# Kernel optimization log

Measured on AMD Instinct MI355X. Metric: run time of the kernel, lower is better.

## Reference

```python
import jax, jax.numpy as jnp
import numpy as np

NUM_LEVELS = 4
RADIUS = 4
B, C, H, W = 2, 256, 96, 96


def _grid_sample_abs(img, grid):
    """Bilinear sample with absolute pixel coords, align_corners=True, zero padding.

    img:  (N, h, w)
    grid: (N, K, K, 2) with last dim = (x, y) absolute pixel coordinates.
    Returns (N, K, K).
    """
    h, w = img.shape[-2:]
    x = grid[..., 0]
    y = grid[..., 1]
    x0 = jnp.floor(x)
    y0 = jnp.floor(y)
    wx1 = x - x0
    wy1 = y - y0
    wx0 = 1.0 - wx1
    wy0 = 1.0 - wy1
    n = jnp.arange(img.shape[0])[:, None, None]

    def gather(xi, yi):
        valid = (xi >= 0) & (xi <= w - 1) & (yi >= 0) & (yi <= h - 1)
        xc = jnp.clip(xi, 0, w - 1).astype(jnp.int32)
        yc = jnp.clip(yi, 0, h - 1).astype(jnp.int32)
        return jnp.where(valid, img[n, yc, xc], 0.0)

    return (gather(x0, y0) * wx0 * wy0
            + gather(x0 + 1, y0) * wx1 * wy0
            + gather(x0, y0 + 1) * wx0 * wy1
            + gather(x0 + 1, y0 + 1) * wx1 * wy1)


def _avg_pool2(x):
    # x: (N, h, w) -> (N, h//2, w//2), kernel 2 stride 2
    n, h, w = x.shape
    return x.reshape(n, h // 2, 2, w // 2, 2).mean(axis=(2, 4))


def setup_inputs() -> dict:
    key = jax.random.key(0)
    k1, k2, k3 = jax.random.split(key, 3)
    fmap1 = jax.random.normal(k1, (B, C, H, W), dtype=jnp.float32)
    fmap2 = jax.random.normal(k2, (B, C, H, W), dtype=jnp.float32)
    # absolute pixel coords (x, y) within the feature map
    centroids_coords = jax.random.uniform(k3, (B, 2, H, W), dtype=jnp.float32) * (W - 1)
    return {"fmap1": fmap1, "fmap2": fmap2, "centroids_coords": centroids_coords}


def reference(fmap1, fmap2, centroids_coords):
    b, c, h, w = fmap1.shape
    # all-pairs dot-product correlation volume: (B, HW, HW)
    f1 = fmap1.reshape(b, c, h * w)
    f2 = fmap2.reshape(b, c, h * w)
    corr = jnp.einsum('bcp,bcq->bpq', f1, f2) / jnp.sqrt(jnp.float32(c))
    corr = corr.reshape(b * h * w, h, w)

    pyramid = [corr]
    for _ in range(NUM_LEVELS - 1):
        corr = _avg_pool2(corr)
        pyramid.append(corr)

    k = 2 * RADIUS + 1
    di = jnp.linspace(-RADIUS, RADIUS, k, dtype=jnp.float32)
    dij = jnp.stack(jnp.meshgrid(di, di, indexing='ij'), axis=-1)  # (k, k, 2)
    delta = dij.reshape(1, k, k, 2)

    cent = centroids_coords.transpose(0, 2, 3, 1).reshape(b * h * w, 1, 1, 2)
    feats = []
    for lvl in pyramid:
        coords = cent + delta                      # (BHW, k, k, 2)
        sampled = _grid_sample_abs(lvl, coords)    # (BHW, k, k)
        feats.append(sampled.reshape(b, h, w, k * k))
        cent = cent / 2

    out = jnp.concatenate(feats, axis=-1)          # (B, H, W, num_levels*k*k)
    return out.transpose(0, 3, 1, 2)
```

## Files before the change

### kernel.cpp

```cpp
#include <hip/hip_runtime.h>
#include <stdint.h>

#define B_ 2
#define C_ 256
#define H_ 96
#define W_ 96
#define HW_ (H_*W_)

typedef _Float16 half8 __attribute__((ext_vector_type(8)));
typedef float f32x4 __attribute__((ext_vector_type(4)));

#define ZPOFF   0u
#define CNTOFF  512u
#define PERMOFF 4096u
#define F1OFF   225280u
#define L0OFF   9662464u
#define L1OFF   19099648u
#define L2OFF   21458944u
#define L3OFF   22048768u
#define SCROFF  22196224u

#define CAP 96
#define DLW 226

__global__ __launch_bounds__(256) void k_tr2(const float* __restrict__ f1,
                                             const float* __restrict__ f2,
                                             _Float16* __restrict__ f1t,
                                             _Float16* __restrict__ L0h) {
  __shared__ float t[32][33];
  const int z = blockIdx.z;
  const int b = z & 1;
  const bool is2 = (z >> 1) != 0;
  const float* in = is2 ? f2 : f1;
  _Float16* out = is2 ? L0h : f1t;
  const float scale = is2 ? 1.0f : 0.0625f;

  const int p0 = blockIdx.x * 32, c0 = blockIdx.y * 32;
  const int tx = threadIdx.x, ty = threadIdx.y;
  const float* src = in + ((size_t)b * C_ + c0) * HW_ + p0;
#pragma unroll
  for (int i = 0; i < 4; ++i)
    t[ty + 8 * i][tx] = src[(size_t)(ty + 8 * i) * HW_ + tx];
  __syncthreads();
  _Float16* dst = out + ((size_t)b * HW_ + p0) * C_ + c0;
#pragma unroll
  for (int i = 0; i < 4; ++i)
    dst[(size_t)(ty + 8 * i) * C_ + tx] = (_Float16)(t[tx][ty + 8 * i] * scale);
}

__global__ __launch_bounds__(256) void k_pool3(const _Float16* __restrict__ L0,
                                               _Float16* __restrict__ L1,
                                               _Float16* __restrict__ L2,
                                               _Float16* __restrict__ L3) {
  int idx = blockIdx.x;
  const int X = idx % 12; idx /= 12;
  const int Y = idx % 12; const int b = idx / 12;
  const int c = threadIdx.x;

  const _Float16* base = L0 + (((size_t)b * 96 + 8 * Y) * 96 + 8 * X) * C_ + c;
  float s1[4][4];
#pragma unroll
  for (int i = 0; i < 4; ++i)
#pragma unroll
    for (int j = 0; j < 4; ++j) {
      const _Float16* p = base + ((size_t)(2 * i) * 96 + 2 * j) * C_;
      s1[i][j] = ((float)p[0] + (float)p[C_] +
                  (float)p[96 * C_] + (float)p[96 * C_ + C_]) * 0.25f;
    }
#pragma unroll
  for (int i = 0; i < 4; ++i)
#pragma unroll
    for (int j = 0; j < 4; ++j)
      L1[(((size_t)b * 48 + 4 * Y + i) * 48 + 4 * X + j) * C_ + c] = (_Float16)s1[i][j];

  float s2[2][2];
#pragma unroll
  for (int i = 0; i < 2; ++i)
#pragma unroll
    for (int j = 0; j < 2; ++j) {
      s2[i][j] = (s1[2 * i][2 * j] + s1[2 * i][2 * j + 1] +
                  s1[2 * i + 1][2 * j] + s1[2 * i + 1][2 * j + 1]) * 0.25f;
      L2[(((size_t)b * 24 + 2 * Y + i) * 24 + 2 * X + j) * C_ + c] = (_Float16)s2[i][j];
    }

  const float s3 = (s2[0][0] + s2[0][1] + s2[1][0] + s2[1][1]) * 0.25f;
  L3[(((size_t)b * 12 + Y) * 12 + X) * C_ + c] = (_Float16)s3;
}

__global__ __launch_bounds__(256) void k_bucket(const float* __restrict__ cent,
                                                int* __restrict__ cnt,
                                                int* __restrict__ perm) {
  const int t = blockIdx.x * 256 + threadIdx.x;
  const int b = t / HW_, yx = t - b * HW_;
  const float cx = cent[(size_t)b * 2 * HW_ + yx];
  const float cy = cent[(size_t)b * 2 * HW_ + HW_ + yx];
  int ci = (int)(cx * 0.125f); ci = min(max(ci, 0), 11);
  int cj = (int)(cy * 0.25f);  cj = min(max(cj, 0), 23);
  const int cell = b * 288 + cj * 12 + ci;
  const int pos = atomicAdd(&cnt[cell], 1);
  if (pos < CAP) perm[cell * CAP + pos] = t;
}

template <int LVL>
__device__ __forceinline__ void cell_level(char* __restrict__ ws,
                                           const float* __restrict__ cent,
                                           int b, int ci, int cj,
                                           const int* __restrict__ pc, int npix,
                                           _Float16* __restrict__ dl,
                                           float* __restrict__ prm, int lane) {
  constexpr int wl = 96 >> LVL;
  constexpr int Wx = (LVL == 0) ? 17 : (LVL == 1) ? 13 : (LVL == 2) ? 11 : 10;
  constexpr int Hy = (LVL == 0) ? 13 : (LVL == 1) ? 11 : 10;
  constexpr int N = Wx * Hy;
  constexpr int ntiles = (N + 15) >> 4;
  constexpr uint32_t LB = (LVL == 0) ? L0OFF : (LVL == 1) ? L1OFF
                        : (LVL == 2) ? L2OFF : L3OFF;
  constexpr uint32_t PBl = (LVL == 0) ? 4718592u : (LVL == 1) ? 1179648u
                         : (LVL == 2) ? 294912u : 73728u;
  constexpr float inv = 1.0f / (float)(1 << LVL);

  const int FXl = (LVL == 0) ? (ci << 3) : (LVL == 1) ? (ci << 2)
                : (LVL == 2) ? (ci << 1) : ci;
  const int FYl = (LVL == 0) ? (cj << 2) : (LVL == 1) ? (cj << 1)
                : (LVL == 2) ? cj : (cj >> 1);
  const int XW0 = FXl - 4, YW0 = FYl - 4;
  const char* lbase = ws + LB + (size_t)b * PBl;
  const char* zp = ws + ZPOFF;
  const char* f1b = ws + F1OFF;
  char* scrb = ws + SCROFF;

  const int row16 = lane & 15, kb = lane >> 4;
  const int nmt = (npix + 47) / 48;

  for (int mt = 0; mt < nmt; ++mt) {
    const int rem = npix - mt * 48;
    const int remc = min(rem, 48);

    half8 av0[8], av1[8], av2[8];
    {
      const int i0 = mt * 48 + row16;
      const int pv0 = (i0 < npix) ? pc[i0] : pc[0];
      const char* a0 = f1b + (size_t)pv0 * 512 + kb * 16;
#pragma unroll
      for (int k = 0; k < 8; ++k) av0[k] = *(const half8*)(a0 + k * 64);
    }
    if (rem > 16) {
      const int i1 = mt * 48 + 16 + row16;
      const int pv1 = (i1 < npix) ? pc[i1] : pc[0];
      const char* a1 = f1b + (size_t)pv1 * 512 + kb * 16;
#pragma unroll
      for (int k = 0; k < 8; ++k) av1[k] = *(const half8*)(a1 + k * 64);
    }
    if (rem > 32) {
      const int i2 = mt * 48 + 32 + row16;
      const int pv2 = (i2 < npix) ? pc[i2] : pc[0];
      const char* a2 = f1b + (size_t)pv2 * 512 + kb * 16;
#pragma unroll
      for (int k = 0; k < 8; ++k) av2[k] = *(const half8*)(a2 + k * 64);
    }

    if (lane < remc) {
      const int pv = pc[mt * 48 + lane];
      const int yx = pv - b * HW_;
      const float cx = cent[(size_t)b * 2 * HW_ + yx];
      const float cy = cent[(size_t)b * 2 * HW_ + HW_ + yx];
      const float cxl = cx * inv, cyl = cy * inv;
      const float fxl = floorf(cxl), fyl = floorf(cyl);
      const int sxp = (int)fxl - FXl, syp = (int)fyl - FYl;
      prm[lane * 4 + 0] = cxl - fxl;
      prm[lane * 4 + 1] = cyl - fyl;
      ((int*)prm)[lane * 4 + 2] = syp * Wx + sxp;
      ((int*)prm)[lane * 4 + 3] = pv;
    }

#pragma unroll
    for (int j = 0; j < ntiles; ++j) {
      const int n = j * 16 + row16;
      const int sy = n / Wx, sx = n - sy * Wx;
      const int gy = YW0 + sy, gx = XW0 + sx;
      const bool val = (n < N) & (gy >= 0) & (gy < wl) & (gx >= 0) & (gx < wl);
      const char* bp = (val ? (lbase + (((size_t)(gy * wl + gx)) << 9)) : zp)
                       + kb * 16;
      half8 bv[8];
#pragma unroll
      for (int k = 0; k < 8; ++k) bv[k] = *(const half8*)(bp + k * 64);

      f32x4 acc0 = {0.f, 0.f, 0.f, 0.f};
#pragma unroll
      for (int k = 0; k < 8; ++k)
        acc0 = __builtin_amdgcn_mfma_f32_16x16x32_f16(av0[k], bv[k], acc0, 0, 0, 0);
      const int col = j * 16 + row16;
#pragma unroll
      for (int j4 = 0; j4 < 4; ++j4)
        dl[(kb * 4 + j4) * DLW + col] = (_Float16)acc0[j4];

      if (rem > 16) {
        f32x4 acc1 = {0.f, 0.f, 0.f, 0.f};
#pragma unroll
        for (int k = 0; k < 8; ++k)
          acc1 = __builtin_amdgcn_mfma_f32_16x16x32_f16(av1[k], bv[k], acc1, 0, 0, 0);
#pragma unroll
        for (int j4 = 0; j4 < 4; ++j4)
          dl[(kb * 4 + j4 + 16) * DLW + col] = (_Float16)acc1[j4];
      }
      if (rem > 32) {
        f32x4 acc2 = {0.f, 0.f, 0.f, 0.f};
#pragma unroll
        for (int k = 0; k < 8; ++k)
          acc2 = __builtin_amdgcn_mfma_f32_16x16x32_f16(av2[k], bv[k], acc2, 0, 0, 0);
#pragma unroll
        for (int j4 = 0; j4 < 4; ++j4)
          dl[(kb * 4 + j4 + 32) * DLW + col] = (_Float16)acc2[j4];
      }
    }

    {
      const int total = remc * 41;
      for (int s = lane; s < total; s += 64) {
        const int p = s / 41;
        const int c = s - p * 41;
        const float wx1 = prm[p * 4 + 0];
        const float wy1 = prm[p * 4 + 1];
        const int n0 = ((const int*)prm)[p * 4 + 2];
        const int pv = ((const int*)prm)[p * 4 + 3];
        const float wx0 = 1.f - wx1, wy0 = 1.f - wy1;
        const _Float16* d = &dl[p * DLW];
        uint32_t packed = 0;
#pragma unroll
        for (int e = 0; e < 2; ++e) {
          const int o = 2 * c + e;
          const int a = o / 9, bq = o - a * 9;
          const int n = n0 + bq * Wx + a;
          const float d00 = (float)d[n],      d10 = (float)d[n + 1];
          const float d01 = (float)d[n + Wx], d11 = (float)d[n + Wx + 1];
          const float v = wy0 * (wx0 * d00 + wx1 * d10) +
                          wy1 * (wx0 * d01 + wx1 * d11);
          const _Float16 h = (_Float16)v;
          packed |= ((uint32_t)*(const uint16_t*)&h) << (16 * e);
        }
        *(uint32_t*)(scrb + (size_t)pv * 656 + LVL * 164 + c * 4) = packed;
      }
    }
  }
}

__global__ __launch_bounds__(64, 2) void k_cell(char* __restrict__ ws,
                                                const float* __restrict__ cent) {
  __shared__ _Float16 dl[48 * DLW];
  __shared__ float prm[48 * 4];

  const int bx = blockIdx.x;
  const int xcd = bx & 7, slot = bx >> 3;
  const int b = xcd >> 2, band = xcd & 3;
  const int lvl = slot / 72;
  const int rem = slot - lvl * 72;
  const int cjb = rem / 12, ci = rem - cjb * 12;
  const int cj = band * 6 + cjb;
  const int cell = b * 288 + cj * 12 + ci;

  const int* cnt = (const int*)(ws + CNTOFF);
  const int npix = min(cnt[cell], CAP);
  if (npix == 0) return;
  const int* pc = (const int*)(ws + PERMOFF) + cell * CAP;

  const int lane = threadIdx.x;
  switch (lvl) {
    case 0: cell_level<0>(ws, cent, b, ci, cj, pc, npix, dl, prm, lane); break;
    case 1: cell_level<1>(ws, cent, b, ci, cj, pc, npix, dl, prm, lane); break;
    case 2: cell_level<2>(ws, cent, b, ci, cj, pc, npix, dl, prm, lane); break;
    default: cell_level<3>(ws, cent, b, ci, cj, pc, npix, dl, prm, lane); break;
  }
}

__global__ __launch_bounds__(256) void k_otrans(const _Float16* __restrict__ scr,
                                                float* __restrict__ out) {
  __shared__ float t[32][33];
  const int b = blockIdx.z;
  const int yx0 = blockIdx.x * 32, c0 = blockIdx.y * 32;
  const int tx = threadIdx.x, ty = threadIdx.y;
#pragma unroll
  for (int i = 0; i < 4; ++i) {
    const int yxi = ty + 8 * i, c = c0 + tx;
    float v = 0.f;
    if (c < 324) {
      const int lv = c / 81, o = c - lv * 81;
      v = (float)scr[((size_t)b * HW_ + yx0 + yxi) * 328 + lv * 82 + o];
    }
    t[yxi][tx] = v;
  }
  __syncthreads();
#pragma unroll
  for (int i = 0; i < 4; ++i) {
    const int c = c0 + ty + 8 * i;
    if (c < 324)
      out[((size_t)b * 324 + c) * HW_ + yx0 + tx] = t[tx][ty + 8 * i];
  }
}

extern "C" void kernel_launch(void* const* d_in, const int* in_sizes, int n_in,
                              void* d_out, int out_size, void* d_ws, size_t ws_size,
                              hipStream_t stream) {
  (void)in_sizes; (void)n_in; (void)out_size; (void)ws_size;
  const float* f1   = (const float*)d_in[0];
  const float* f2   = (const float*)d_in[1];
  const float* cent = (const float*)d_in[2];
  float* out = (float*)d_out;

  char* ws = (char*)d_ws;
  _Float16* f1t = (_Float16*)(ws + F1OFF);
  _Float16* L0  = (_Float16*)(ws + L0OFF);
  _Float16* L1  = (_Float16*)(ws + L1OFF);
  _Float16* L2  = (_Float16*)(ws + L2OFF);
  _Float16* L3  = (_Float16*)(ws + L3OFF);
  int* cnt  = (int*)(ws + CNTOFF);
  int* perm = (int*)(ws + PERMOFF);

  (void)hipMemsetAsync(ws, 0, 4096, stream);

  hipLaunchKernelGGL(k_bucket, dim3(72), dim3(256), 0, stream, cent, cnt, perm);

  dim3 tb(32, 8, 1);
  hipLaunchKernelGGL(k_tr2, dim3(HW_ / 32, C_ / 32, 2 * B_), tb, 0, stream,
                     f1, f2, f1t, L0);
  hipLaunchKernelGGL(k_pool3, dim3(B_ * 12 * 12), dim3(256), 0, stream,
                     L0, L1, L2, L3);

  hipLaunchKernelGGL(k_cell, dim3(2304), dim3(64), 0, stream, ws, cent);

  hipLaunchKernelGGL(k_otrans, dim3(HW_ / 32, 11, B_), tb, 0, stream,
                     (const _Float16*)(ws + SCROFF), out);
}
```

Before: 81.76 us.

## Split cell kernel MFMA tiles across two wavefronts per block

Each cell block now runs two wavefronts instead of one. They split the window tiles by parity, and barriers separate the MFMA stage from the bilinear interpolation stage. The interpolation loop is spread over 128 threads. The aim is to double the parallelism per cell so latency from global loads and MFMA chains is better hidden. In exchange, both waves redundantly load the A fragments, and the added __syncthreads calls may reduce occupancy per block.

```diff
diff --git a/kernel.cpp b/kernel.cpp
--- a/kernel.cpp
+++ b/kernel.cpp
@@ -107,7 +107,7 @@
                                            int b, int ci, int cj,
                                            const int* __restrict__ pc, int npix,
                                            _Float16* __restrict__ dl,
-                                           float* __restrict__ prm, int lane) {
+                                           float* __restrict__ prm, int tid) {
   constexpr int wl = 96 >> LVL;
   constexpr int Wx = (LVL == 0) ? 17 : (LVL == 1) ? 13 : (LVL == 2) ? 11 : 10;
   constexpr int Hy = (LVL == 0) ? 13 : (LVL == 1) ? 11 : 10;
@@ -129,6 +129,7 @@
   const char* f1b = ws + F1OFF;
   char* scrb = ws + SCROFF;
 
+  const int lane = tid & 63, wv = tid >> 6;
   const int row16 = lane & 15, kb = lane >> 4;
   const int nmt = (npix + 47) / 48;
 
@@ -159,22 +160,23 @@
       for (int k = 0; k < 8; ++k) av2[k] = *(const half8*)(a2 + k * 64);
     }
 
-    if (lane < remc) {
-      const int pv = pc[mt * 48 + lane];
+    if (tid < remc) {
+      const int pv = pc[mt * 48 + tid];
       const int yx = pv - b * HW_;
       const float cx = cent[(size_t)b * 2 * HW_ + yx];
       const float cy = cent[(size_t)b * 2 * HW_ + HW_ + yx];
       const float cxl = cx * inv, cyl = cy * inv;
       const float fxl = floorf(cxl), fyl = floorf(cyl);
       const int sxp = (int)fxl - FXl, syp = (int)fyl - FYl;
-      prm[lane * 4 + 0] = cxl - fxl;
-      prm[lane * 4 + 1] = cyl - fyl;
-      ((int*)prm)[lane * 4 + 2] = syp * Wx + sxp;
-      ((int*)prm)[lane * 4 + 3] = pv;
+      prm[tid * 4 + 0] = cxl - fxl;
+      prm[tid * 4 + 1] = cyl - fyl;
+      ((int*)prm)[tid * 4 + 2] = syp * Wx + sxp;
+      ((int*)prm)[tid * 4 + 3] = pv;
     }
 
 #pragma unroll
     for (int j = 0; j < ntiles; ++j) {
+      if ((j & 1) != wv) continue;
       const int n = j * 16 + row16;
       const int sy = n / Wx, sx = n - sy * Wx;
       const int gy = YW0 + sy, gx = XW0 + sx;
@@ -213,10 +215,11 @@
           dl[(kb * 4 + j4 + 32) * DLW + col] = (_Float16)acc2[j4];
       }
     }
+    __syncthreads();
 
     {
       const int total = remc * 41;
-      for (int s = lane; s < total; s += 64) {
+      for (int s = tid; s < total; s += 128) {
         const int p = s / 41;
         const int c = s - p * 41;
         const float wx1 = prm[p * 4 + 0];
@@ -241,11 +244,12 @@
         *(uint32_t*)(scrb + (size_t)pv * 656 + LVL * 164 + c * 4) = packed;
       }
     }
+    if (mt + 1 < nmt) __syncthreads();
   }
 }
 
-__global__ __launch_bounds__(64, 2) void k_cell(char* __restrict__ ws,
-                                                const float* __restrict__ cent) {
+__global__ __launch_bounds__(128, 2) void k_cell(char* __restrict__ ws,
+                                                 const float* __restrict__ cent) {
   __shared__ _Float16 dl[48 * DLW];
   __shared__ float prm[48 * 4];
 
@@ -263,12 +267,12 @@
   if (npix == 0) return;
   const int* pc = (const int*)(ws + PERMOFF) + cell * CAP;
 
-  const int lane = threadIdx.x;
+  const int tid = threadIdx.x;
   switch (lvl) {
-    case 0: cell_level<0>(ws, cent, b, ci, cj, pc, npix, dl, prm, lane); break;
-    case 1: cell_level<1>(ws, cent, b, ci, cj, pc, npix, dl, prm, lane); break;
-    case 2: cell_level<2>(ws, cent, b, ci, cj, pc, npix, dl, prm, lane); break;
-    default: cell_level<3>(ws, cent, b, ci, cj, pc, npix, dl, prm, lane); break;
+    case 0: cell_level<0>(ws, cent, b, ci, cj, pc, npix, dl, prm, tid); break;
+    case 1: cell_level<1>(ws, cent, b, ci, cj, pc, npix, dl, prm, tid); break;
+    case 2: cell_level<2>(ws, cent, b, ci, cj, pc, npix, dl, prm, tid); break;
+    default: cell_level<3>(ws, cent, b, ci, cj, pc, npix, dl, prm, tid); break;
   }
 }
 
@@ -325,7 +329,7 @@
   hipLaunchKernelGGL(k_pool3, dim3(B_ * 12 * 12), dim3(256), 0, stream,
                      L0, L1, L2, L3);
 
-  hipLaunchKernelGGL(k_cell, dim3(2304), dim3(64), 0, stream, ws, cent);
+  hipLaunchKernelGGL(k_cell, dim3(2304), dim3(128), 0, stream, ws, cent);
 
   hipLaunchKernelGGL(k_otrans, dim3(HW_ / 32, 11, B_), tb, 0, stream,
                      (const _Float16*)(ws + SCROFF), out);
```

After: 82.59 us. About the same (+1.0%).

## Fold bucketing into pool kernel and process level pairs per cell block

Applied to the files above, without the earlier changes.

The standalone bucketing kernel is merged into k_pool3, which removes one kernel launch and its dependency step. k_cell now processes two pyramid levels per block, pairing 0 with 3 and 1 with 2. The fmap1 A-fragments loaded into registers are reused across both levels, and the grid shrinks from 2304 to 1152 blocks. The trade-off is fewer blocks to hide latency and longer per-block work, with the level pairing chosen to balance the load between blocks.

```diff
diff --git a/kernel.cpp b/kernel.cpp
--- a/kernel.cpp
+++ b/kernel.cpp
@@ -51,7 +51,24 @@
 __global__ __launch_bounds__(256) void k_pool3(const _Float16* __restrict__ L0,
                                                _Float16* __restrict__ L1,
                                                _Float16* __restrict__ L2,
-                                               _Float16* __restrict__ L3) {
+                                               _Float16* __restrict__ L3,
+                                               const float* __restrict__ cent,
+                                               int* __restrict__ cnt,
+                                               int* __restrict__ perm) {
+  {
+    const int t = blockIdx.x * 256 + threadIdx.x;
+    if (t < B_ * HW_) {
+      const int b = t / HW_, yx = t - b * HW_;
+      const float cx = cent[(size_t)b * 2 * HW_ + yx];
+      const float cy = cent[(size_t)b * 2 * HW_ + HW_ + yx];
+      int ci = (int)(cx * 0.125f); ci = min(max(ci, 0), 11);
+      int cj = (int)(cy * 0.25f);  cj = min(max(cj, 0), 23);
+      const int cell = b * 288 + cj * 12 + ci;
+      const int pos = atomicAdd(&cnt[cell], 1);
+      if (pos < CAP) perm[cell * CAP + pos] = t;
+    }
+  }
+
   int idx = blockIdx.x;
   const int X = idx % 12; idx /= 12;
   const int Y = idx % 12; const int b = idx / 12;
@@ -87,27 +104,17 @@
   L3[(((size_t)b * 12 + Y) * 12 + X) * C_ + c] = (_Float16)s3;
 }
 
-__global__ __launch_bounds__(256) void k_bucket(const float* __restrict__ cent,
-                                                int* __restrict__ cnt,
-                                                int* __restrict__ perm) {
-  const int t = blockIdx.x * 256 + threadIdx.x;
-  const int b = t / HW_, yx = t - b * HW_;
-  const float cx = cent[(size_t)b * 2 * HW_ + yx];
-  const float cy = cent[(size_t)b * 2 * HW_ + HW_ + yx];
-  int ci = (int)(cx * 0.125f); ci = min(max(ci, 0), 11);
-  int cj = (int)(cy * 0.25f);  cj = min(max(cj, 0), 23);
-  const int cell = b * 288 + cj * 12 + ci;
-  const int pos = atomicAdd(&cnt[cell], 1);
-  if (pos < CAP) perm[cell * CAP + pos] = t;
-}
-
 template <int LVL>
-__device__ __forceinline__ void cell_level(char* __restrict__ ws,
-                                           const float* __restrict__ cent,
-                                           int b, int ci, int cj,
-                                           const int* __restrict__ pc, int npix,
-                                           _Float16* __restrict__ dl,
-                                           float* __restrict__ prm, int lane) {
+__device__ __forceinline__ void do_level(char* __restrict__ ws,
+                                         const float* __restrict__ cent,
+                                         int b, int ci, int cj,
+                                         const int* __restrict__ pc, int npix,
+                                         int mt, int rem,
+                                         const half8 (&av0)[8],
+                                         const half8 (&av1)[8],
+                                         const half8 (&av2)[8],
+                                         _Float16* __restrict__ dl,
+                                         float* __restrict__ prm, int lane) {
   constexpr int wl = 96 >> LVL;
   constexpr int Wx = (LVL == 0) ? 17 : (LVL == 1) ? 13 : (LVL == 2) ? 11 : 10;
   constexpr int Hy = (LVL == 0) ? 13 : (LVL == 1) ? 11 : 10;
@@ -126,15 +133,121 @@
   const int XW0 = FXl - 4, YW0 = FYl - 4;
   const char* lbase = ws + LB + (size_t)b * PBl;
   const char* zp = ws + ZPOFF;
+  char* scrb = ws + SCROFF;
+
+  const int row16 = lane & 15, kb = lane >> 4;
+  const int remc = min(rem, 48);
+
+  if (lane < remc) {
+    const int pv = pc[mt * 48 + lane];
+    const int yx = pv - b * HW_;
+    const float cx = cent[(size_t)b * 2 * HW_ + yx];
+    const float cy = cent[(size_t)b * 2 * HW_ + HW_ + yx];
+    const float cxl = cx * inv, cyl = cy * inv;
+    const float fxl = floorf(cxl), fyl = floorf(cyl);
+    const int sxp = (int)fxl - FXl, syp = (int)fyl - FYl;
+    prm[lane * 4 + 0] = cxl - fxl;
+    prm[lane * 4 + 1] = cyl - fyl;
+    ((int*)prm)[lane * 4 + 2] = syp * Wx + sxp;
+    ((int*)prm)[lane * 4 + 3] = pv;
+  }
+
+#pragma unroll
+  for (int j = 0; j < ntiles; ++j) {
+    const int n = j * 16 + row16;
+    const int sy = n / Wx, sx = n - sy * Wx;
+    const int gy = YW0 + sy, gx = XW0 + sx;
+    const bool val = (n < N) & (gy >= 0) & (gy < wl) & (gx >= 0) & (gx < wl);
+    const char* bp = (val ? (lbase + (((size_t)(gy * wl + gx)) << 9)) : zp)
+                     + kb * 16;
+    half8 bv[8];
+#pragma unroll
+    for (int k = 0; k < 8; ++k) bv[k] = *(const half8*)(bp + k * 64);
+
+    f32x4 acc0 = {0.f, 0.f, 0.f, 0.f};
+#pragma unroll
+    for (int k = 0; k < 8; ++k)
+      acc0 = __builtin_amdgcn_mfma_f32_16x16x32_f16(av0[k], bv[k], acc0, 0, 0, 0);
+    const int col = j * 16 + row16;
+#pragma unroll
+    for (int j4 = 0; j4 < 4; ++j4)
+      dl[(kb * 4 + j4) * DLW + col] = (_Float16)acc0[j4];
+
+    if (rem > 16) {
+      f32x4 acc1 = {0.f, 0.f, 0.f, 0.f};
+#pragma unroll
+      for (int k = 0; k < 8; ++k)
+        acc1 = __builtin_amdgcn_mfma_f32_16x16x32_f16(av1[k], bv[k], acc1, 0, 0, 0);
+#pragma unroll
+      for (int j4 = 0; j4 < 4; ++j4)
+        dl[(kb * 4 + j4 + 16) * DLW + col] = (_Float16)acc1[j4];
+    }
+    if (rem > 32) {
+      f32x4 acc2 = {0.f, 0.f, 0.f, 0.f};
+#pragma unroll
+      for (int k = 0; k < 8; ++k)
+        acc2 = __builtin_amdgcn_mfma_f32_16x16x32_f16(av2[k], bv[k], acc2, 0, 0, 0);
+#pragma unroll
+      for (int j4 = 0; j4 < 4; ++j4)
+        dl[(kb * 4 + j4 + 32) * DLW + col] = (_Float16)acc2[j4];
+    }
+  }
+
+  {
+    const int total = remc * 41;
+    for (int s = lane; s < total; s += 64) {
+      const int p = s / 41;
+      const int c = s - p * 41;
+      const float wx1 = prm[p * 4 + 0];
+      const float wy1 = prm[p * 4 + 1];
+      const int n0 = ((const int*)prm)[p * 4 + 2];
+      const int pv = ((const int*)prm)[p * 4 + 3];
+      const float wx0 = 1.f - wx1, wy0 = 1.f - wy1;
+      const _Float16* d = &dl[p * DLW];
+      uint32_t packed = 0;
+#pragma unroll
+      for (int e = 0; e < 2; ++e) {
+        const int o = 2 * c + e;
+        const int a = o / 9, bq = o - a * 9;
+        const int n = n0 + bq * Wx + a;
+        const float d00 = (float)d[n],      d10 = (float)d[n + 1];
+        const float d01 = (float)d[n + Wx], d11 = (float)d[n + Wx + 1];
+        const float v = wy0 * (wx0 * d00 + wx1 * d10) +
+                        wy1 * (wx0 * d01 + wx1 * d11);
+        const _Float16 h = (_Float16)v;
+        packed |= ((uint32_t)*(const uint16_t*)&h) << (16 * e);
+      }
+      *(uint32_t*)(scrb + (size_t)pv * 656 + LVL * 164 + c * 4) = packed;
+    }
+  }
+}
+
+__global__ __launch_bounds__(64, 2) void k_cell(char* __restrict__ ws,
+                                                const float* __restrict__ cent) {
+  __shared__ _Float16 dl[48 * DLW];
+  __shared__ float prm[48 * 4];
+
+  const int bx = blockIdx.x;
+  const int xcd = bx & 7, slot = bx >> 3;
+  const int b = xcd >> 2, band = xcd & 3;
+  const int pair = slot / 72;
+  const int rem2 = slot - pair * 72;
+  const int cjb = rem2 / 12, ci = rem2 - cjb * 12;
+  const int cj = band * 6 + cjb;
+  const int cell = b * 288 + cj * 12 + ci;
+
+  const int* cnt = (const int*)(ws + CNTOFF);
+  const int npix = min(cnt[cell], CAP);
+  if (npix == 0) return;
+  const int* pc = (const int*)(ws + PERMOFF) + cell * CAP;
+
+  const int lane = threadIdx.x;
+  const int row16 = lane & 15, kb = lane >> 4;
   const char* f1b = ws + F1OFF;
-  char* scrb = ws + SCROFF;
-
-  const int row16 = lane & 15, kb = lane >> 4;
   const int nmt = (npix + 47) / 48;
 
   for (int mt = 0; mt < nmt; ++mt) {
     const int rem = npix - mt * 48;
-    const int remc = min(rem, 48);
 
     half8 av0[8], av1[8], av2[8];
     {
@@ -159,116 +272,13 @@
       for (int k = 0; k < 8; ++k) av2[k] = *(const half8*)(a2 + k * 64);
     }
 
-    if (lane < remc) {
-      const int pv = pc[mt * 48 + lane];
-      const int yx = pv - b * HW_;
-      const float cx = cent[(size_t)b * 2 * HW_ + yx];
-      const float cy = cent[(size_t)b * 2 * HW_ + HW_ + yx];
-      const float cxl = cx * inv, cyl = cy * inv;
-      const float fxl = floorf(cxl), fyl = floorf(cyl);
-      const int sxp = (int)fxl - FXl, syp = (int)fyl - FYl;
-      prm[lane * 4 + 0] = cxl - fxl;
-      prm[lane * 4 + 1] = cyl - fyl;
-      ((int*)prm)[lane * 4 + 2] = syp * Wx + sxp;
-      ((int*)prm)[lane * 4 + 3] = pv;
-    }
-
-#pragma unroll
-    for (int j = 0; j < ntiles; ++j) {
-      const int n = j * 16 + row16;
-      const int sy = n / Wx, sx = n - sy * Wx;
-      const int gy = YW0 + sy, gx = XW0 + sx;
-      const bool val = (n < N) & (gy >= 0) & (gy < wl) & (gx >= 0) & (gx < wl);
-      const char* bp = (val ? (lbase + (((size_t)(gy * wl + gx)) << 9)) : zp)
-                       + kb * 16;
-      half8 bv[8];
-#pragma unroll
-      for (int k = 0; k < 8; ++k) bv[k] = *(const half8*)(bp + k * 64);
-
-      f32x4 acc0 = {0.f, 0.f, 0.f, 0.f};
-#pragma unroll
-      for (int k = 0; k < 8; ++k)
-        acc0 = __builtin_amdgcn_mfma_f32_16x16x32_f16(av0[k], bv[k], acc0, 0, 0, 0);
-      const int col = j * 16 + row16;
-#pragma unroll
-      for (int j4 = 0; j4 < 4; ++j4)
-        dl[(kb * 4 + j4) * DLW + col] = (_Float16)acc0[j4];
-
-      if (rem > 16) {
-        f32x4 acc1 = {0.f, 0.f, 0.f, 0.f};
-#pragma unroll
-        for (int k = 0; k < 8; ++k)
-          acc1 = __builtin_amdgcn_mfma_f32_16x16x32_f16(av1[k], bv[k], acc1, 0, 0, 0);
-#pragma unroll
-        for (int j4 = 0; j4 < 4; ++j4)
-          dl[(kb * 4 + j4 + 16) * DLW + col] = (_Float16)acc1[j4];
-      }
-      if (rem > 32) {
-        f32x4 acc2 = {0.f, 0.f, 0.f, 0.f};
-#pragma unroll
-        for (int k = 0; k < 8; ++k)
-          acc2 = __builtin_amdgcn_mfma_f32_16x16x32_f16(av2[k], bv[k], acc2, 0, 0, 0);
-#pragma unroll
-        for (int j4 = 0; j4 < 4; ++j4)
-          dl[(kb * 4 + j4 + 32) * DLW + col] = (_Float16)acc2[j4];
-      }
-    }
-
-    {
-      const int total = remc * 41;
-      for (int s = lane; s < total; s += 64) {
-        const int p = s / 41;
-        const int c = s - p * 41;
-        const float wx1 = prm[p * 4 + 0];
-        const float wy1 = prm[p * 4 + 1];
-        const int n0 = ((const int*)prm)[p * 4 + 2];
-        const int pv = ((const int*)prm)[p * 4 + 3];
-        const float wx0 = 1.f - wx1, wy0 = 1.f - wy1;
-        const _Float16* d = &dl[p * DLW];
-        uint32_t packed = 0;
-#pragma unroll
-        for (int e = 0; e < 2; ++e) {
-          const int o = 2 * c + e;
-          const int a = o / 9, bq = o - a * 9;
-          const int n = n0 + bq * Wx + a;
-          const float d00 = (float)d[n],      d10 = (float)d[n + 1];
-          const float d01 = (float)d[n + Wx], d11 = (float)d[n + Wx + 1];
-          const float v = wy0 * (wx0 * d00 + wx1 * d10) +
-                          wy1 * (wx0 * d01 + wx1 * d11);
-          const _Float16 h = (_Float16)v;
-          packed |= ((uint32_t)*(const uint16_t*)&h) << (16 * e);
-        }
-        *(uint32_t*)(scrb + (size_t)pv * 656 + LVL * 164 + c * 4) = packed;
-      }
-    }
-  }
-}
-
-__global__ __launch_bounds__(64, 2) void k_cell(char* __restrict__ ws,
-                                                const float* __restrict__ cent) {
-  __shared__ _Float16 dl[48 * DLW];
-  __shared__ float prm[48 * 4];
-
-  const int bx = blockIdx.x;
-  const int xcd = bx & 7, slot = bx >> 3;
-  const int b = xcd >> 2, band = xcd & 3;
-  const int lvl = slot / 72;
-  const int rem = slot - lvl * 72;
-  const int cjb = rem / 12, ci = rem - cjb * 12;
-  const int cj = band * 6 + cjb;
-  const int cell = b * 288 + cj * 12 + ci;
-
-  const int* cnt = (const int*)(ws + CNTOFF);
-  const int npix = min(cnt[cell], CAP);
-  if (npix == 0) return;
-  const int* pc = (const int*)(ws + PERMOFF) + cell * CAP;
-
-  const int lane = threadIdx.x;
-  switch (lvl) {
-    case 0: cell_level<0>(ws, cent, b, ci, cj, pc, npix, dl, prm, lane); break;
-    case 1: cell_level<1>(ws, cent, b, ci, cj, pc, npix, dl, prm, lane); break;
-    case 2: cell_level<2>(ws, cent, b, ci, cj, pc, npix, dl, prm, lane); break;
-    default: cell_level<3>(ws, cent, b, ci, cj, pc, npix, dl, prm, lane); break;
+    if (pair == 0) {
+      do_level<0>(ws, cent, b, ci, cj, pc, npix, mt, rem, av0, av1, av2, dl, prm, lane);
+      do_level<3>(ws, cent, b, ci, cj, pc, npix, mt, rem, av0, av1, av2, dl, prm, lane);
+    } else {
+      do_level<1>(ws, cent, b, ci, cj, pc, npix, mt, rem, av0, av1, av2, dl, prm, lane);
+      do_level<2>(ws, cent, b, ci, cj, pc, npix, mt, rem, av0, av1, av2, dl, prm, lane);
+    }
   }
 }
 
@@ -317,15 +327,13 @@
 
   (void)hipMemsetAsync(ws, 0, 4096, stream);
 
-  hipLaunchKernelGGL(k_bucket, dim3(72), dim3(256), 0, stream, cent, cnt, perm);
-
   dim3 tb(32, 8, 1);
   hipLaunchKernelGGL(k_tr2, dim3(HW_ / 32, C_ / 32, 2 * B_), tb, 0, stream,
                      f1, f2, f1t, L0);
   hipLaunchKernelGGL(k_pool3, dim3(B_ * 12 * 12), dim3(256), 0, stream,
-                     L0, L1, L2, L3);
-
-  hipLaunchKernelGGL(k_cell, dim3(2304), dim3(64), 0, stream, ws, cent);
+                     L0, L1, L2, L3, cent, cnt, perm);
+
+  hipLaunchKernelGGL(k_cell, dim3(1152), dim3(64), 0, stream, ws, cent);
 
   hipLaunchKernelGGL(k_otrans, dim3(HW_ / 32, 11, B_), tb, 0, stream,
                      (const _Float16*)(ws + SCROFF), out);
```

After: 89.14 us. 1.09x slower.
